# Kernel tuning notes

Measured on AMD Instinct MI355X. Metric: run time of the kernel, lower is better.

## Reference

```python
import jax, jax.numpy as jnp
import numpy as np

HIDDEN = 1024
INTER = 4096
N_EXPERTS = 8
TOP_K = 2
INIT_STD = 0.02


def setup_inputs() -> dict:
    key = jax.random.key(0)
    ks = jax.random.split(key, 6)
    x = jax.random.normal(ks[0], (2, 1024, HIDDEN), dtype=jnp.float32)
    Wg = jax.random.normal(ks[1], (N_EXPERTS, HIDDEN), dtype=jnp.float32) * INIT_STD
    # Expert MLP params, stacked over experts. W1: [E, H, I], W2: [E, I, H].
    W1 = jax.random.normal(ks[2], (N_EXPERTS, HIDDEN, INTER), dtype=jnp.float32) * INIT_STD
    b1 = jnp.zeros((N_EXPERTS, INTER), dtype=jnp.float32)
    W2 = jax.random.normal(ks[3], (N_EXPERTS, INTER, HIDDEN), dtype=jnp.float32) * INIT_STD
    b2 = jnp.zeros((N_EXPERTS, HIDDEN), dtype=jnp.float32)
    return {"x": x, "Wg": Wg, "W1": W1, "b1": b1, "W2": W2, "b2": b2}


def reference(x, Wg, W1, b1, W2, b2):
    orig_shape = x.shape
    xt = x.reshape(-1, HIDDEN)              # [T, H]
    T = xt.shape[0]

    # Gating: top-k logits -> softmax over the k selected experts.
    logits = xt @ Wg.T                      # [T, E]
    topk_logits, topk_idx = jax.lax.top_k(logits, TOP_K)   # [T, K]
    w = jax.nn.softmax(topk_logits, axis=-1)               # [T, K]

    # Scatter top-k weights into a dense [T, E] gate matrix (zeros elsewhere).
    rows = jnp.arange(T)[:, None]
    gates = jnp.zeros((T, N_EXPERTS), xt.dtype).at[rows, topk_idx].add(w)

    # Dense expert compute (mathematically identical: non-selected experts get
    # gate weight 0). Expert MLP: Linear -> GELU (exact, erf) -> Linear.
    h = jnp.einsum('th,ehi->tei', xt, W1) + b1             # [T, E, I]
    h = jax.nn.gelu(h, approximate=False)
    o = jnp.einsum('tei,eih->teh', h, W2) + b2             # [T, E, H]
    y = jnp.einsum('te,teh->th', gates, o)                 # [T, H]
    return y.reshape(orig_shape)
```

## Files before the change

### kernel.cpp

```cpp
#include <hip/hip_runtime.h>
#include <hip/hip_bf16.h>

#define HID 1024
#define INTER 4096
#define NE 8
#define NTOK 2048
#define MAXROWS 5120

typedef __attribute__((ext_vector_type(8))) short short8v;
typedef __attribute__((ext_vector_type(4))) float f32x4;

__device__ __forceinline__ unsigned short f2bf(float f) {
  unsigned int u = __builtin_bit_cast(unsigned int, f);
  u = (u + 0x7FFFu + ((u >> 16) & 1u)) >> 16;
  return (unsigned short)u;
}

typedef const __attribute__((address_space(1))) unsigned int* gas_t;
typedef __attribute__((address_space(3))) unsigned int* las_t;
__device__ __forceinline__ void gld16(const unsigned short* g, unsigned short* l) {
  __builtin_amdgcn_global_load_lds((gas_t)(const void*)g, (las_t)(void*)l, 16, 0, 0);
}

__global__ __launch_bounds__(256) void convx_kernel(const float* __restrict__ in,
                                                    unsigned short* __restrict__ out) {
  size_t i = (size_t)blockIdx.x * 256 + threadIdx.x;
  f32x4 v = *(const f32x4*)&in[i * 4];
  uint2 r;
  r.x = (unsigned int)f2bf(v[0]) | ((unsigned int)f2bf(v[1]) << 16);
  r.y = (unsigned int)f2bf(v[2]) | ((unsigned int)f2bf(v[3]) << 16);
  *(uint2*)&out[i * 4] = r;
}

__global__ __launch_bounds__(256) void tconv_kernel(const float* __restrict__ in,
                                                    unsigned short* __restrict__ out,
                                                    int R, int C) {
  __shared__ float t[64][65];
  const int z = blockIdx.z;
  const int r0 = blockIdx.y * 64, c0 = blockIdx.x * 64;
  const int tr = threadIdx.x / 16;
  const int tc = (threadIdx.x % 16) * 4;
  const float* ip = in + ((size_t)z * R + r0) * (size_t)C + c0;
#pragma unroll
  for (int p = 0; p < 4; ++p) {
    f32x4 v = *(const f32x4*)&ip[(size_t)(p * 16 + tr) * C + tc];
    t[p * 16 + tr][tc + 0] = v[0];
    t[p * 16 + tr][tc + 1] = v[1];
    t[p * 16 + tr][tc + 2] = v[2];
    t[p * 16 + tr][tc + 3] = v[3];
  }
  __syncthreads();
  unsigned short* op = out + ((size_t)z * C + c0) * (size_t)R + r0;
#pragma unroll
  for (int p = 0; p < 4; ++p) {
    int c = p * 16 + tr;
    unsigned int a0 = (unsigned int)f2bf(t[tc + 0][c]) | ((unsigned int)f2bf(t[tc + 1][c]) << 16);
    unsigned int a1 = (unsigned int)f2bf(t[tc + 2][c]) | ((unsigned int)f2bf(t[tc + 3][c]) << 16);
    uint2 val; val.x = a0; val.y = a1;
    *(uint2*)&op[(size_t)c * R + tc] = val;
  }
}

__global__ __launch_bounds__(256) void gating_kernel(const float* __restrict__ x,
                                                     const float* __restrict__ wg,
                                                     int* __restrict__ tok_e,
                                                     float* __restrict__ tok_w) {
  const int t = blockIdx.x;
  float acc[NE];
#pragma unroll
  for (int e = 0; e < NE; ++e) acc[e] = 0.f;
  for (int k = threadIdx.x; k < HID; k += 256) {
    float xv = x[(size_t)t * HID + k];
#pragma unroll
    for (int e = 0; e < NE; ++e) acc[e] += xv * wg[e * HID + k];
  }
#pragma unroll
  for (int e = 0; e < NE; ++e) {
#pragma unroll
    for (int off = 32; off >= 1; off >>= 1) acc[e] += __shfl_xor(acc[e], off, 64);
  }
  __shared__ float red[4][NE];
  const int wave = threadIdx.x >> 6, lane = threadIdx.x & 63;
  if (lane == 0) {
#pragma unroll
    for (int e = 0; e < NE; ++e) red[wave][e] = acc[e];
  }
  __syncthreads();
  if (threadIdx.x == 0) {
    float l[NE];
#pragma unroll
    for (int e = 0; e < NE; ++e) l[e] = red[0][e] + red[1][e] + red[2][e] + red[3][e];
    int i0 = 0;
#pragma unroll
    for (int e = 1; e < NE; ++e) if (l[e] > l[i0]) i0 = e;
    int i1 = -1;
#pragma unroll
    for (int e = 0; e < NE; ++e) {
      if (e == i0) continue;
      if (i1 < 0 || l[e] > l[i1]) i1 = e;
    }
    float e1 = __expf(l[i1] - l[i0]);
    float w0 = 1.f / (1.f + e1);
    tok_e[t * 2 + 0] = i0;
    tok_e[t * 2 + 1] = i1;
    tok_w[t * 2 + 0] = w0;
    tok_w[t * 2 + 1] = 1.f - w0;
  }
}

__global__ __launch_bounds__(512) void routing_kernel(const int* __restrict__ tok_e,
                                                      int* __restrict__ list_tok,
                                                      int* __restrict__ tok_gslot,
                                                      int* __restrict__ offs_out) {
  __shared__ int cnts[NE];
  __shared__ int offs_s[NE + 1];
  const int e = threadIdx.x >> 6, lane = threadIdx.x & 63;
  int c = 0;
  for (int base = 0; base < NTOK; base += 64) {
    int tok = base + lane;
    int e0 = tok_e[tok * 2], e1 = tok_e[tok * 2 + 1];
    bool m = (e0 == e) || (e1 == e);
    unsigned long long mask = __ballot(m);
    c += __popcll(mask);
  }
  if (lane == 0) cnts[e] = c;
  __syncthreads();
  if (threadIdx.x == 0) {
    int o = 0;
    for (int i = 0; i < NE; ++i) { offs_s[i] = o; o += (cnts[i] + 127) & ~127; }
    offs_s[NE] = o;
    for (int i = 0; i <= NE; ++i) offs_out[i] = offs_s[i];
  }
  __syncthreads();
  const int off = offs_s[e];
  int run = 0;
  for (int base = 0; base < NTOK; base += 64) {
    int tok = base + lane;
    int e0 = tok_e[tok * 2], e1 = tok_e[tok * 2 + 1];
    bool m = (e0 == e) || (e1 == e);
    unsigned long long mask = __ballot(m);
    int pos = run + __popcll(mask & ((1ull << lane) - 1ull));
    if (m) {
      int gs = off + pos;
      list_tok[gs] = tok;
      tok_gslot[tok * 2 + ((e0 == e) ? 0 : 1)] = gs;
    }
    run += __popcll(mask);
  }
  const int cnt = cnts[e];
  const int padded = (cnt + 127) & ~127;
  for (int p = cnt + lane; p < padded; p += 64) list_tok[off + p] = 0;
}

template <int KTOT, int NTOT, bool FIRST, int NSPLIT>
__global__ __launch_bounds__(256, 3) void moe_gemm(const unsigned short* __restrict__ Abase,
                                                   const unsigned short* __restrict__ Bbase,
                                                   const float* __restrict__ bias,
                                                   const int* __restrict__ list_tok,
                                                   const int* __restrict__ offs,
                                                   void* __restrict__ outp) {
  constexpr int KS = KTOT / NSPLIT;
  constexpr int NT = KS / 32;
  constexpr int nM = MAXROWS / 128;
  constexpr int nN = NTOT / 128;
  __shared__ __align__(16) unsigned short lds[3][2][4096];

  const int nwg = nN * nM * NSPLIT;
  int wg = blockIdx.x;
  wg = (wg & 7) * (nwg >> 3) + (wg >> 3);
  const int ks = (NSPLIT > 1) ? (wg / (nM * nN)) : 0;
  const int rem = wg % (nM * nN);
  const int mt = rem % nM;
  const int nt = rem / nM;
  const int grow0 = mt * 128;
  if (grow0 >= offs[NE]) return;
  int e = 0;
#pragma unroll
  for (int i = 1; i < NE; ++i) if (grow0 >= offs[i]) e = i;
  const int n0 = nt * 128;
  const int k0 = ks * KS;

  const int tid = threadIdx.x;
  const int wave = tid >> 6, lane = tid & 63;

  const int srow = tid >> 2;
  const int skc = (((tid & 3) ^ ((srow >> 1) & 3)) * 8);
  const unsigned short* ag[2];
  const unsigned short* bg[2];
#pragma unroll
  for (int j = 0; j < 2; ++j) {
    const int row = srow + j * 64;
    size_t arow;
    if (FIRST) arow = (size_t)list_tok[grow0 + row] * KTOT;
    else       arow = (size_t)(grow0 + row) * KTOT;
    ag[j] = Abase + arow + k0 + skc;
    bg[j] = Bbase + (size_t)e * NTOT * KTOT + (size_t)(n0 + row) * KTOT + k0 + skc;
  }
  const int wbase = wave * 512;

  const int wm = wave >> 1, wn = wave & 1;
  const int fr = lane & 15;
  const int q = lane >> 4;
  int aoff[4], boff[4];
#pragma unroll
  for (int m = 0; m < 4; ++m) {
    const int row = wm * 64 + m * 16 + fr;
    aoff[m] = row * 32 + ((q ^ ((row >> 1) & 3)) * 8);
  }
#pragma unroll
  for (int n = 0; n < 4; ++n) {
    const int row = wn * 64 + n * 16 + fr;
    boff[n] = row * 32 + ((q ^ ((row >> 1) & 3)) * 8);
  }

  f32x4 acc[4][4] = {};

#define STAGE(S, SLOT)                                             \
  {                                                                \
    gld16(ag[0] + (S) * 32, &lds[SLOT][0][wbase]);                 \
    gld16(ag[1] + (S) * 32, &lds[SLOT][0][wbase + 2048]);          \
    gld16(bg[0] + (S) * 32, &lds[SLOT][1][wbase]);                 \
    gld16(bg[1] + (S) * 32, &lds[SLOT][1][wbase + 2048]);          \
  }

#define KITER(S, SL, DO_STAGE, VMSTR)                              \
  {                                                                \
    asm volatile("s_waitcnt vmcnt(" VMSTR ")" ::: "memory");       \
    asm volatile("s_barrier" ::: "memory");                        \
    const unsigned short* A = &lds[SL][0][0];                      \
    const unsigned short* B = &lds[SL][1][0];                      \
    short8v af[4];                                                 \
    _Pragma("unroll")                                              \
    for (int m = 0; m < 4; ++m) af[m] = *(const short8v*)&A[aoff[m]]; \
    if (DO_STAGE) {                                                \
      int s2 = (SL) + 2; if (s2 >= 3) s2 -= 3;                     \
      STAGE((S) + 2, s2);                                          \
    }                                                              \
    __builtin_amdgcn_s_setprio(1);                                 \
    _Pragma("unroll")                                              \
    for (int n = 0; n < 4; ++n) {                                  \
      short8v bf = *(const short8v*)&B[boff[n]];                   \
      _Pragma("unroll")                                            \
      for (int m = 0; m < 4; ++m)                                  \
        acc[m][n] = __builtin_amdgcn_mfma_f32_16x16x32_bf16(af[m], bf, acc[m][n], 0, 0, 0); \
    }                                                              \
    __builtin_amdgcn_s_setprio(0);                                 \
  }

  STAGE(0, 0);
  STAGE(1, 1);

  int sl = 0;
  for (int s = 0; s < NT - 2; ++s) {
    KITER(s, sl, true, "4");
    sl = sl + 1; if (sl >= 3) sl = 0;
  }
  KITER(NT - 2, sl, false, "4");
  sl = sl + 1; if (sl >= 3) sl = 0;
  KITER(NT - 1, sl, false, "0");

#undef KITER
#undef STAGE

  const int r4 = lane >> 4;
#pragma unroll
  for (int m = 0; m < 4; ++m) {
#pragma unroll
    for (int n = 0; n < 4; ++n) {
      const int gcol = n0 + wn * 64 + n * 16 + fr;
      float bv = 0.f;
      if (FIRST) bv = bias[e * NTOT + gcol];
#pragma unroll
      for (int r = 0; r < 4; ++r) {
        const int grow = grow0 + wm * 64 + m * 16 + r4 * 4 + r;
        float v = acc[m][n][r] + bv;
        if (FIRST) {
          v = 0.5f * v * (1.0f + erff(v * 0.70710678118654752f));
          ((unsigned short*)outp)[(size_t)grow * NTOT + gcol] = f2bf(v);
        } else {
          ((float*)outp)[((size_t)ks * MAXROWS + grow) * NTOT + gcol] = v;
        }
      }
    }
  }
}

__global__ __launch_bounds__(256) void combine_kernel(const float* __restrict__ part,
                                                      const int* __restrict__ tok_gslot,
                                                      const int* __restrict__ tok_e,
                                                      const float* __restrict__ tok_w,
                                                      const float* __restrict__ b2,
                                                      float* __restrict__ y) {
  const int t = blockIdx.x;
  const int c = threadIdx.x * 4;
  const int gs0 = tok_gslot[t * 2 + 0], gs1 = tok_gslot[t * 2 + 1];
  const int e0 = tok_e[t * 2 + 0], e1 = tok_e[t * 2 + 1];
  const float w0 = tok_w[t * 2 + 0], w1 = tok_w[t * 2 + 1];
  const size_t P1 = (size_t)MAXROWS * HID;
  f32x4 a0 = *(const f32x4*)&part[(size_t)gs0 * HID + c];
  f32x4 a1 = *(const f32x4*)&part[P1 + (size_t)gs0 * HID + c];
  f32x4 d0 = *(const f32x4*)&part[(size_t)gs1 * HID + c];
  f32x4 d1 = *(const f32x4*)&part[P1 + (size_t)gs1 * HID + c];
  f32x4 bb0 = *(const f32x4*)&b2[e0 * HID + c];
  f32x4 bb1 = *(const f32x4*)&b2[e1 * HID + c];
  f32x4 r;
#pragma unroll
  for (int i = 0; i < 4; ++i)
    r[i] = w0 * (a0[i] + a1[i] + bb0[i]) + w1 * (d0[i] + d1[i] + bb1[i]);
  *(f32x4*)&y[(size_t)t * HID + c] = r;
}

extern "C" void kernel_launch(void* const* d_in, const int* in_sizes, int n_in,
                              void* d_out, int out_size, void* d_ws, size_t ws_size,
                              hipStream_t stream) {
  const float* x  = (const float*)d_in[0];
  const float* wg = (const float*)d_in[1];
  const float* W1 = (const float*)d_in[2];
  const float* b1 = (const float*)d_in[3];
  const float* W2 = (const float*)d_in[4];
  const float* b2 = (const float*)d_in[5];
  float* y = (float*)d_out;

  unsigned char* ws = (unsigned char*)d_ws;
  size_t off = 0;
  unsigned short* w1t = (unsigned short*)(ws + off);
  float* part         = (float*)(ws + off);          off += (size_t)NE * HID * INTER * 2;
  unsigned short* w2t = (unsigned short*)(ws + off); off += (size_t)NE * INTER * HID * 2;
  unsigned short* xb  = (unsigned short*)(ws + off); off += (size_t)NTOK * HID * 2;
  unsigned short* h   = (unsigned short*)(ws + off); off += (size_t)MAXROWS * INTER * 2;
  int* tok_e          = (int*)(ws + off);            off += NTOK * 2 * 4;
  float* tok_w        = (float*)(ws + off);          off += NTOK * 2 * 4;
  int* tok_gslot      = (int*)(ws + off);            off += NTOK * 2 * 4;
  int* list_tok       = (int*)(ws + off);            off += MAXROWS * 4;
  int* offs           = (int*)(ws + off);            off += 64;
  (void)ws_size; (void)in_sizes; (void)n_in; (void)out_size;

  convx_kernel<<<(NTOK * HID / 4 + 255) / 256, 256, 0, stream>>>(x, xb);
  tconv_kernel<<<dim3(INTER / 64, HID / 64, NE), 256, 0, stream>>>(W1, w1t, HID, INTER);
  tconv_kernel<<<dim3(HID / 64, INTER / 64, NE), 256, 0, stream>>>(W2, w2t, INTER, HID);
  gating_kernel<<<NTOK, 256, 0, stream>>>(x, wg, tok_e, tok_w);
  routing_kernel<<<1, 512, 0, stream>>>(tok_e, list_tok, tok_gslot, offs);
  moe_gemm<HID, INTER, true, 1><<<(INTER / 128) * (MAXROWS / 128), 256, 0, stream>>>(
      xb, w1t, b1, list_tok, offs, (void*)h);
  moe_gemm<INTER, HID, false, 2><<<(HID / 128) * (MAXROWS / 128) * 2, 256, 0, stream>>>(
      h, w2t, b2, list_tok, offs, (void*)part);
  combine_kernel<<<NTOK, 256, 0, stream>>>(part, tok_gslot, tok_e, tok_w, b2, y);
}
```

Before: 253.5 us.

## Store second-GEMM split-K partials as bf16, raise split to 4, batch B-fragment loads

The second expert GEMM now writes its split-K partial sums as bf16 instead of fp32, and the split-K factor goes from 2 to 4 so the launch has twice as many blocks. The combine kernel is templated on the split count and sums the bf16 partials in fp32. Inside the k-loop, all four B fragments are read from LDS before the next stage is issued, rather than being read one at a time between MFMAs. This aims to halve partial-buffer traffic and improve occupancy and latency hiding, at the cost of extra rounding on the partials and more combine reads.

```diff
diff --git a/kernel.cpp b/kernel.cpp
--- a/kernel.cpp
+++ b/kernel.cpp
@@ -8,12 +8,17 @@
 #define MAXROWS 5120
 
 typedef __attribute__((ext_vector_type(8))) short short8v;
+typedef __attribute__((ext_vector_type(4))) short short4v;
 typedef __attribute__((ext_vector_type(4))) float f32x4;
 
 __device__ __forceinline__ unsigned short f2bf(float f) {
   unsigned int u = __builtin_bit_cast(unsigned int, f);
   u = (u + 0x7FFFu + ((u >> 16) & 1u)) >> 16;
   return (unsigned short)u;
+}
+__device__ __forceinline__ float bf2f(unsigned short s) {
+  unsigned int u = ((unsigned int)s) << 16;
+  return __builtin_bit_cast(float, u);
 }
 
 typedef const __attribute__((address_space(1))) unsigned int* gas_t;
@@ -223,28 +228,28 @@
     gld16(bg[1] + (S) * 32, &lds[SLOT][1][wbase + 2048]);          \
   }
 
-#define KITER(S, SL, DO_STAGE, VMSTR)                              \
-  {                                                                \
-    asm volatile("s_waitcnt vmcnt(" VMSTR ")" ::: "memory");       \
-    asm volatile("s_barrier" ::: "memory");                        \
-    const unsigned short* A = &lds[SL][0][0];                      \
-    const unsigned short* B = &lds[SL][1][0];                      \
-    short8v af[4];                                                 \
-    _Pragma("unroll")                                              \
+#define KITER(S, SL, DO_STAGE, VMSTR)                                 \
+  {                                                                   \
+    asm volatile("s_waitcnt vmcnt(" VMSTR ")" ::: "memory");          \
+    asm volatile("s_barrier" ::: "memory");                           \
+    const unsigned short* A = &lds[SL][0][0];                         \
+    const unsigned short* B = &lds[SL][1][0];                         \
+    short8v af[4], bf[4];                                             \
+    _Pragma("unroll")                                                 \
     for (int m = 0; m < 4; ++m) af[m] = *(const short8v*)&A[aoff[m]]; \
-    if (DO_STAGE) {                                                \
-      int s2 = (SL) + 2; if (s2 >= 3) s2 -= 3;                     \
-      STAGE((S) + 2, s2);                                          \
-    }                                                              \
-    __builtin_amdgcn_s_setprio(1);                                 \
-    _Pragma("unroll")                                              \
-    for (int n = 0; n < 4; ++n) {                                  \
-      short8v bf = *(const short8v*)&B[boff[n]];                   \
-      _Pragma("unroll")                                            \
-      for (int m = 0; m < 4; ++m)                                  \
-        acc[m][n] = __builtin_amdgcn_mfma_f32_16x16x32_bf16(af[m], bf, acc[m][n], 0, 0, 0); \
-    }                                                              \
-    __builtin_amdgcn_s_setprio(0);                                 \
+    _Pragma("unroll")                                                 \
+    for (int n = 0; n < 4; ++n) bf[n] = *(const short8v*)&B[boff[n]]; \
+    if (DO_STAGE) {                                                   \
+      int s2 = (SL) + 2; if (s2 >= 3) s2 -= 3;                        \
+      STAGE((S) + 2, s2);                                             \
+    }                                                                 \
+    __builtin_amdgcn_s_setprio(1);                                    \
+    _Pragma("unroll")                                                 \
+    for (int n = 0; n < 4; ++n)                                       \
+      _Pragma("unroll")                                               \
+      for (int m = 0; m < 4; ++m)                                     \
+        acc[m][n] = __builtin_amdgcn_mfma_f32_16x16x32_bf16(af[m], bf[n], acc[m][n], 0, 0, 0); \
+    __builtin_amdgcn_s_setprio(0);                                    \
   }
 
   STAGE(0, 0);
@@ -278,14 +283,15 @@
           v = 0.5f * v * (1.0f + erff(v * 0.70710678118654752f));
           ((unsigned short*)outp)[(size_t)grow * NTOT + gcol] = f2bf(v);
         } else {
-          ((float*)outp)[((size_t)ks * MAXROWS + grow) * NTOT + gcol] = v;
+          ((unsigned short*)outp)[((size_t)ks * MAXROWS + grow) * NTOT + gcol] = f2bf(v);
         }
       }
     }
   }
 }
 
-__global__ __launch_bounds__(256) void combine_kernel(const float* __restrict__ part,
+template <int NSPLIT>
+__global__ __launch_bounds__(256) void combine_kernel(const unsigned short* __restrict__ part,
                                                       const int* __restrict__ tok_gslot,
                                                       const int* __restrict__ tok_e,
                                                       const float* __restrict__ tok_w,
@@ -296,17 +302,23 @@
   const int gs0 = tok_gslot[t * 2 + 0], gs1 = tok_gslot[t * 2 + 1];
   const int e0 = tok_e[t * 2 + 0], e1 = tok_e[t * 2 + 1];
   const float w0 = tok_w[t * 2 + 0], w1 = tok_w[t * 2 + 1];
-  const size_t P1 = (size_t)MAXROWS * HID;
-  f32x4 a0 = *(const f32x4*)&part[(size_t)gs0 * HID + c];
-  f32x4 a1 = *(const f32x4*)&part[P1 + (size_t)gs0 * HID + c];
-  f32x4 d0 = *(const f32x4*)&part[(size_t)gs1 * HID + c];
-  f32x4 d1 = *(const f32x4*)&part[P1 + (size_t)gs1 * HID + c];
+  float s0[4] = {0.f, 0.f, 0.f, 0.f}, s1[4] = {0.f, 0.f, 0.f, 0.f};
+#pragma unroll
+  for (int ks = 0; ks < NSPLIT; ++ks) {
+    short4v p0 = *(const short4v*)&part[((size_t)ks * MAXROWS + gs0) * HID + c];
+    short4v p1 = *(const short4v*)&part[((size_t)ks * MAXROWS + gs1) * HID + c];
+#pragma unroll
+    for (int i = 0; i < 4; ++i) {
+      s0[i] += bf2f((unsigned short)p0[i]);
+      s1[i] += bf2f((unsigned short)p1[i]);
+    }
+  }
   f32x4 bb0 = *(const f32x4*)&b2[e0 * HID + c];
   f32x4 bb1 = *(const f32x4*)&b2[e1 * HID + c];
   f32x4 r;
 #pragma unroll
   for (int i = 0; i < 4; ++i)
-    r[i] = w0 * (a0[i] + a1[i] + bb0[i]) + w1 * (d0[i] + d1[i] + bb1[i]);
+    r[i] = w0 * (s0[i] + bb0[i]) + w1 * (s1[i] + bb1[i]);
   *(f32x4*)&y[(size_t)t * HID + c] = r;
 }
 
@@ -323,16 +335,16 @@
 
   unsigned char* ws = (unsigned char*)d_ws;
   size_t off = 0;
-  unsigned short* w1t = (unsigned short*)(ws + off);
-  float* part         = (float*)(ws + off);          off += (size_t)NE * HID * INTER * 2;
-  unsigned short* w2t = (unsigned short*)(ws + off); off += (size_t)NE * INTER * HID * 2;
-  unsigned short* xb  = (unsigned short*)(ws + off); off += (size_t)NTOK * HID * 2;
-  unsigned short* h   = (unsigned short*)(ws + off); off += (size_t)MAXROWS * INTER * 2;
-  int* tok_e          = (int*)(ws + off);            off += NTOK * 2 * 4;
-  float* tok_w        = (float*)(ws + off);          off += NTOK * 2 * 4;
-  int* tok_gslot      = (int*)(ws + off);            off += NTOK * 2 * 4;
-  int* list_tok       = (int*)(ws + off);            off += MAXROWS * 4;
-  int* offs           = (int*)(ws + off);            off += 64;
+  unsigned short* w1t  = (unsigned short*)(ws + off);
+  unsigned short* part = (unsigned short*)(ws + off); off += (size_t)NE * HID * INTER * 2;
+  unsigned short* w2t  = (unsigned short*)(ws + off); off += (size_t)NE * INTER * HID * 2;
+  unsigned short* xb   = (unsigned short*)(ws + off); off += (size_t)NTOK * HID * 2;
+  unsigned short* h    = (unsigned short*)(ws + off); off += (size_t)MAXROWS * INTER * 2;
+  int* tok_e           = (int*)(ws + off);            off += NTOK * 2 * 4;
+  float* tok_w         = (float*)(ws + off);          off += NTOK * 2 * 4;
+  int* tok_gslot       = (int*)(ws + off);            off += NTOK * 2 * 4;
+  int* list_tok        = (int*)(ws + off);            off += MAXROWS * 4;
+  int* offs            = (int*)(ws + off);            off += 64;
   (void)ws_size; (void)in_sizes; (void)n_in; (void)out_size;
 
   convx_kernel<<<(NTOK * HID / 4 + 255) / 256, 256, 0, stream>>>(x, xb);
@@ -342,7 +354,7 @@
   routing_kernel<<<1, 512, 0, stream>>>(tok_e, list_tok, tok_gslot, offs);
   moe_gemm<HID, INTER, true, 1><<<(INTER / 128) * (MAXROWS / 128), 256, 0, stream>>>(
       xb, w1t, b1, list_tok, offs, (void*)h);
-  moe_gemm<INTER, HID, false, 2><<<(HID / 128) * (MAXROWS / 128) * 2, 256, 0, stream>>>(
+  moe_gemm<INTER, HID, false, 4><<<(HID / 128) * (MAXROWS / 128) * 4, 256, 0, stream>>>(
       h, w2t, b2, list_tok, offs, (void*)part);
-  combine_kernel<<<NTOK, 256, 0, stream>>>(part, tok_gslot, tok_e, tok_w, b2, y);
-}
+  combine_kernel<4><<<NTOK, 256, 0, stream>>>(part, tok_gslot, tok_e, tok_w, b2, y);
+}
```

New measurement: 250.9 us. About the same (-1.1%).
